# Kernel optimization log

Measured on AMD Instinct MI355X. Metric: run time of the kernel, lower is better.

Reference implementation:

```python
import jax, jax.numpy as jnp
import numpy as np

N_NODES = 50000
N_EDGES = 1600000
IN_FEAT = 128
OUT_FEAT = 128
NUM_RELS = 16
NUM_BASES = 4


def setup_inputs() -> dict:
    key = jax.random.key(0)
    ks = jax.random.split(key, 7)
    x = jax.random.normal(ks[0], (N_NODES, IN_FEAT), dtype=jnp.float32)
    W_bases = jax.random.normal(ks[1], (NUM_BASES, IN_FEAT, OUT_FEAT), dtype=jnp.float32) * (1.0 / np.sqrt(IN_FEAT))
    w_comp = jax.random.normal(ks[2], (NUM_RELS, NUM_BASES), dtype=jnp.float32)
    norm = jax.random.uniform(ks[3], (N_EDGES, 1), dtype=jnp.float32)
    src = jax.random.randint(ks[4], (N_EDGES,), 0, N_NODES, dtype=jnp.int32)
    dst = jax.random.randint(ks[5], (N_EDGES,), 0, N_NODES, dtype=jnp.int32)
    etype = jax.random.randint(ks[6], (N_EDGES,), 0, NUM_RELS, dtype=jnp.int32)
    return {"x": x, "W_bases": W_bases, "w_comp": w_comp, "norm": norm,
            "src": src, "dst": dst, "etype": etype}


def _combine_weights(W_bases, w_comp):
    # Faithful to the torch code: stack -> permute(1,0,2) -> matmul -> view(-1, out) -> split(in_feat)
    # [B, in, out] -> [in, B, out]
    Wb = jnp.transpose(W_bases, (1, 0, 2))
    # [R, B] @ [in, B, out] (batched over 'in') -> [in, R, out]
    W = jnp.matmul(w_comp, Wb)
    # view(-1, out) then split into chunks of in_feat rows == reshape(R, in, out)
    return W.reshape(-1, OUT_FEAT).reshape(NUM_RELS, IN_FEAT, OUT_FEAT)


def reference(x, W_bases, w_comp, norm, src, dst, etype):
    # per-relation weights [R, in, out]
    W = _combine_weights(W_bases, w_comp)
    # src_mul_edge: gather source node features, scale by per-edge norm  [E, in]
    msg = x[src] * norm
    # 'sum' aggregation per (relation, dst-node) segment  -> [R, N, in]
    seg = etype.astype(jnp.int32) * N_NODES + dst.astype(jnp.int32)
    agg = jax.ops.segment_sum(msg, seg, num_segments=NUM_RELS * N_NODES)
    agg = agg.reshape(NUM_RELS, N_NODES, IN_FEAT)
    # per-relation mm then merge across relation subgraphs with node_reduce 'sum'  -> [N, out]
    out = jnp.einsum('rni,rio->no', agg, W)
    # bias=None, activation=None in this configuration
    return out
```

## Files before the change

kernel.cpp:

```cpp
#include <hip/hip_runtime.h>


#define N_NODES  50000
#define N_EDGES  1600000
#define IN_FEAT  128
#define OUT_FEAT 128
#define NUM_RELS 16
#define NUM_BASES 4
#define XC_K     32
#define BIN_CAP  96
#define NPB      16
#define RS       516
#define ACCF_WORDS 8704

#define OFF_CNT      0
#define OFF_SPILLCNT 200000
#define OFF_SPILL    200064
#define OFF_BINS     6600064
#define OFF_XC       45000064
#define WS_NEED      51400064

__global__ __launch_bounds__(256) void prep(
    const float* __restrict__ x, const float* __restrict__ w_comp,
    const int* __restrict__ src, const int* __restrict__ dst,
    const int* __restrict__ etype, const float* __restrict__ norm,
    float* __restrict__ xc, int* __restrict__ cnt, uint2* __restrict__ bins,
    int* __restrict__ spillcnt, int* __restrict__ spill)
{
  {
    const int lane = threadIdx.x & 31;
    const int grp  = threadIdx.x >> 5;
    const int j = lane & 7;
    const int b = lane >> 3;
    float wc[16];
    #pragma unroll
    for (int t = 0; t < 16; ++t) wc[t] = w_comp[t * NUM_BASES + b];
    for (int n = blockIdx.x * 8 + grp; n < N_NODES; n += 2048 * 8) {
      const float4* xr = (const float4*)(x + (size_t)n * IN_FEAT) + j * 4;
      float acc = 0.f;
      #pragma unroll
      for (int q = 0; q < 4; ++q) {
        float4 v = xr[q];
        acc += v.x * wc[q*4+0] + v.y * wc[q*4+1]
             + v.z * wc[q*4+2] + v.w * wc[q*4+3];
      }
      xc[n * XC_K + lane] = acc;
    }
  }
  {
    const int e4 = (blockIdx.x * 256 + threadIdx.x) * 4;
    if (e4 < N_EDGES) {
      const int4   s4 = *(const int4*)&src[e4];
      const int4   d4 = *(const int4*)&dst[e4];
      const int4   t4 = *(const int4*)&etype[e4];
      const float4 n4 = *(const float4*)&norm[e4];
      const int   ss[4] = {s4.x, s4.y, s4.z, s4.w};
      const int   dd[4] = {d4.x, d4.y, d4.z, d4.w};
      const int   tt[4] = {t4.x, t4.y, t4.z, t4.w};
      const float nn[4] = {n4.x, n4.y, n4.z, n4.w};
      #pragma unroll
      for (int q = 0; q < 4; ++q) {
        const int pos = atomicAdd(&cnt[dd[q]], 1);
        if (pos < BIN_CAP) {
          bins[(size_t)dd[q] * BIN_CAP + pos] =
              make_uint2((unsigned)ss[q] | ((unsigned)tt[q] << 17),
                         __float_as_uint(nn[q]));
        } else {
          const int k = atomicAdd(spillcnt, 1);
          if (k < N_EDGES) spill[k] = e4 + q;
        }
      }
    }
  }
}

__device__ inline void red_write(float* accf, int slot, float4 (&ac)[4][2]) {
  const int base = slot * 34;
  #pragma unroll
  for (int nn = 0; nn < 4; ++nn) {
    *(float2*)&accf[base + nn*8 + 0] = make_float2(ac[nn][0].x, ac[nn][0].y);
    *(float2*)&accf[base + nn*8 + 2] = make_float2(ac[nn][0].z, ac[nn][0].w);
    *(float2*)&accf[base + nn*8 + 4] = make_float2(ac[nn][1].x, ac[nn][1].y);
    *(float2*)&accf[base + nn*8 + 6] = make_float2(ac[nn][1].z, ac[nn][1].w);
  }
}
__device__ inline void red_read(const float* accf, int slot, float4 (&ac)[4][2]) {
  const int base = slot * 34;
  #pragma unroll
  for (int nn = 0; nn < 4; ++nn) {
    float2 v0 = *(const float2*)&accf[base + nn*8 + 0];
    float2 v1 = *(const float2*)&accf[base + nn*8 + 2];
    float2 v2 = *(const float2*)&accf[base + nn*8 + 4];
    float2 v3 = *(const float2*)&accf[base + nn*8 + 6];
    ac[nn][0].x += v0.x; ac[nn][0].y += v0.y;
    ac[nn][0].z += v1.x; ac[nn][0].w += v1.y;
    ac[nn][1].x += v2.x; ac[nn][1].y += v2.y;
    ac[nn][1].z += v3.x; ac[nn][1].w += v3.y;
  }
}

__device__ inline float selb(const float4& v, int bb) {
  return bb == 0 ? v.x : bb == 1 ? v.y : bb == 2 ? v.z : v.w;
}

__global__ __launch_bounds__(512, 8) void rgcn_fused(
    const int* __restrict__ cnt, const uint2* __restrict__ bins,
    const float* __restrict__ xc, const float* __restrict__ Wb,
    float* __restrict__ out)
{
  __shared__ float accf[ACCF_WORDS];

  const int t    = threadIdx.x;
  const int w    = t >> 6;
  const int lane = t & 63;
  const int h    = lane >> 5;
  const int l5   = lane & 31;
  const int perm = (l5 & 7) * 4 + (l5 >> 3);

  for (int i = t; i < ACCF_WORDS / 4; i += 512)
    ((float4*)accf)[i] = make_float4(0.f, 0.f, 0.f, 0.f);
  __syncthreads();

  const int nodeBase = blockIdx.x * NPB;
  const int ln = w * 2 + h;
  const int n  = nodeBase + ln;
  int c = cnt[n]; c = c > BIN_CAP ? BIN_CAP : c;
  const int cmax   = max(c, __shfl_xor(c, 32));
  const int npairs = (cmax + 1) >> 1;

  const uint4* bp4 = (const uint4*)(bins + (size_t)n * BIN_CAP);
  const int awb = ln * RS + perm;

  uint4 q0 = bp4[0];
  int s00 = (0 < c) ? (int)(q0.x & 0x1FFFF) : 0;
  int s01 = (1 < c) ? (int)(q0.z & 0x1FFFF) : 0;
  float xa = xc[(size_t)s00 * XC_K + l5];
  float xb = xc[(size_t)s01 * XC_K + l5];
  uint4 q1 = bp4[1];

  for (int p = 0; p < npairs; ++p) {
    const int i0 = 2 * (p + 1);
    const int s10 = (i0     < c) ? (int)(q1.x & 0x1FFFF) : 0;
    const int s11 = (i0 + 1 < c) ? (int)(q1.z & 0x1FFFF) : 0;
    const float ya = xc[(size_t)s10 * XC_K + l5];
    const float yb = xc[(size_t)s11 * XC_K + l5];
    const uint4 q2 = bp4[p + 2];
    const int e0 = 2 * p;
    const float v0 = (e0     < c) ? xa * __uint_as_float(q0.y) : 0.f;
    const float v1 = (e0 + 1 < c) ? xb * __uint_as_float(q0.w) : 0.f;
    const int et0 = (int)((q0.x >> 17) & 15);
    const int et1 = (int)((q0.z >> 17) & 15);
    accf[awb + et0 * 32] += v0;
    accf[awb + et1 * 32] += v1;
    q0 = q1; q1 = q2; xa = ya; xb = yb;
  }
  __syncthreads();

  const int ks = w;
  const int ng = lane & 3;
  const int og = lane >> 2;
  const float* wbase = Wb + og * 8;

  float4 ac[4][2];
  #pragma unroll
  for (int nn = 0; nn < 4; ++nn) {
    ac[nn][0] = make_float4(0.f, 0.f, 0.f, 0.f);
    ac[nn][1] = make_float4(0.f, 0.f, 0.f, 0.f);
  }

  #pragma unroll 4
  for (int q = 0; q < 16; ++q) {
    const int k0 = ks * 64 + q * 4;
    const int r0 = (k0 >> 5) * 8 + ((k0 >> 2) & 7);
    float4 a4[4];
    #pragma unroll
    for (int nn = 0; nn < 4; ++nn)
      a4[nn] = *(const float4*)&accf[(ng * 4 + nn) * RS + k0];
    #pragma unroll
    for (int bb = 0; bb < 4; ++bb) {
      const float* wr = wbase + (size_t)(bb * 128 + r0) * 128;
      const float4 w0 = *(const float4*)wr;
      const float4 w1 = *(const float4*)(wr + 4);
      #pragma unroll
      for (int nn = 0; nn < 4; ++nn) {
        const float s = selb(a4[nn], bb);
        ac[nn][0].x += s * w0.x; ac[nn][0].y += s * w0.y;
        ac[nn][0].z += s * w0.z; ac[nn][0].w += s * w0.w;
        ac[nn][1].x += s * w1.x; ac[nn][1].y += s * w1.y;
        ac[nn][1].z += s * w1.z; ac[nn][1].w += s * w1.w;
      }
    }
  }

  __syncthreads();
  if (ks >= 4)             red_write(accf, (ks - 4) * 64 + lane, ac);
  __syncthreads();
  if (ks < 4)              red_read (accf, ks * 64 + lane, ac);
  __syncthreads();
  if (ks == 2 || ks == 3)  red_write(accf, (ks - 2) * 64 + lane, ac);
  __syncthreads();
  if (ks < 2)              red_read (accf, ks * 64 + lane, ac);
  __syncthreads();
  if (ks == 1)             red_write(accf, lane, ac);
  __syncthreads();
  if (ks == 0) {
    red_read(accf, lane, ac);
    #pragma unroll
    for (int nn = 0; nn < 4; ++nn) {
      const int node = nodeBase + ng * 4 + nn;
      *(float4*)(out + (size_t)node * OUT_FEAT + og * 8)     = ac[nn][0];
      *(float4*)(out + (size_t)node * OUT_FEAT + og * 8 + 4) = ac[nn][1];
    }
  }
}

__global__ __launch_bounds__(256) void spill_fix(
    const int* __restrict__ spillcnt, const int* __restrict__ spill,
    const float* __restrict__ xc, const float* __restrict__ Wb,
    const float* __restrict__ norm, const int* __restrict__ src,
    const int* __restrict__ dst, const int* __restrict__ etype,
    float* __restrict__ out)
{
  int cntv = *spillcnt; if (cntv > N_EDGES) cntv = N_EDGES;
  for (int idx = blockIdx.x * blockDim.x + threadIdx.x; idx < cntv;
       idx += gridDim.x * blockDim.x) {
    const int e = spill[idx];
    const int s = src[e], d = dst[e], et = etype[e];
    const float nm = norm[e];
    float m[32];
    #pragma unroll
    for (int l = 0; l < 32; ++l) m[l] = xc[(size_t)s * XC_K + l] * nm;
    for (int o = 0; o < OUT_FEAT; ++o) {
      float a = 0.f;
      #pragma unroll
      for (int l = 0; l < 32; ++l)
        a += m[l] * Wb[(size_t)((l >> 3) * 128 + et * 8 + (l & 7)) * OUT_FEAT + o];
      atomicAdd(&out[(size_t)d * OUT_FEAT + o], a);
    }
  }
}

__global__ __launch_bounds__(256) void edge_direct(
    const float* __restrict__ x, const float* __restrict__ W_bases,
    const float* __restrict__ w_comp, const float* __restrict__ norm,
    const int* __restrict__ src, const int* __restrict__ dst,
    const int* __restrict__ etype, float* __restrict__ out)
{
  const int wave = threadIdx.x >> 6;
  const int lane = threadIdx.x & 63;
  const int j = lane & 7;
  const int b = (lane >> 3) & 3;
  float wc[16];
  #pragma unroll
  for (int t = 0; t < 16; ++t) wc[t] = w_comp[t * NUM_BASES + b];
  for (int e = blockIdx.x * 4 + wave; e < N_EDGES; e += gridDim.x * 4) {
    const int s = src[e], d = dst[e], et = etype[e];
    const float nm = norm[e];
    const float4* xr = (const float4*)(x + (size_t)s * IN_FEAT) + j * 4;
    float m = 0.f;
    #pragma unroll
    for (int q = 0; q < 4; ++q) {
      float4 v = xr[q];
      m += v.x * wc[q*4+0] + v.y * wc[q*4+1]
         + v.z * wc[q*4+2] + v.w * wc[q*4+3];
    }
    m *= nm;
    float acc0 = 0.f, acc1 = 0.f;
    #pragma unroll
    for (int p = 0; p < 32; ++p) {
      float mv = __shfl(m, p, 64);
      const float* Wr = W_bases + (size_t)((p >> 3) * 128 + et * 8 + (p & 7)) * OUT_FEAT;
      acc0 += mv * Wr[lane];
      acc1 += mv * Wr[64 + lane];
    }
    atomicAdd(out + (size_t)d * OUT_FEAT + lane, acc0);
    atomicAdd(out + (size_t)d * OUT_FEAT + 64 + lane, acc1);
  }
}

extern "C" void kernel_launch(void* const* d_in, const int* in_sizes, int n_in,
                              void* d_out, int out_size, void* d_ws, size_t ws_size,
                              hipStream_t stream) {
  const float* x       = (const float*)d_in[0];
  const float* W_bases = (const float*)d_in[1];
  const float* w_comp  = (const float*)d_in[2];
  const float* norm    = (const float*)d_in[3];
  const int*   src     = (const int*)d_in[4];
  const int*   dst     = (const int*)d_in[5];
  const int*   etype   = (const int*)d_in[6];
  float* out = (float*)d_out;

  if (ws_size >= (size_t)WS_NEED) {
    char* ws = (char*)d_ws;
    int*   cntp     = (int*)(ws + OFF_CNT);
    int*   spillcnt = (int*)(ws + OFF_SPILLCNT);
    int*   spill    = (int*)(ws + OFF_SPILL);
    uint2* bins     = (uint2*)(ws + OFF_BINS);
    float* xc       = (float*)(ws + OFF_XC);

    hipMemsetAsync(cntp, 0, 200064, stream);
    prep<<<2048, 256, 0, stream>>>(x, w_comp, src, dst, etype, norm,
                                   xc, cntp, bins, spillcnt, spill);
    rgcn_fused<<<N_NODES / NPB, 512, 0, stream>>>(cntp, bins, xc, W_bases, out);
    spill_fix<<<16, 256, 0, stream>>>(spillcnt, spill, xc, W_bases,
                                      norm, src, dst, etype, out);
  } else {
    hipMemsetAsync(out, 0, (size_t)out_size * sizeof(float), stream);
    edge_direct<<<8192, 256, 0, stream>>>(x, W_bases, w_comp, norm,
                                          src, dst, etype, out);
  }
}
```

Measured before the change: 451.8 us.

## Split prep into separate kernels and deepen edge gather pipeline to four edges

The combined prep kernel is split into a node-precompute kernel with one block per 8 nodes and a separate edge-binning kernel, so each has a right-sized grid instead of one 2048-block grid with a grid-stride loop. The per-node edge loop in the fused kernel now handles four edges per iteration with a one-group lookahead, issuing four xc gathers at a time to hide memory latency. Source indices are clamped to valid nodes rather than masked by count. The cost is an extra kernel launch, more registers in the fused kernel, and extra bin reads past the count.

```diff
diff --git a/kernel.cpp b/kernel.cpp
--- a/kernel.cpp
+++ b/kernel.cpp
@@ -20,55 +20,57 @@
 #define OFF_XC       45000064
 #define WS_NEED      51400064
 
-__global__ __launch_bounds__(256) void prep(
+__global__ __launch_bounds__(256) void precomp_k(
     const float* __restrict__ x, const float* __restrict__ w_comp,
+    float* __restrict__ xc)
+{
+  const int lane = threadIdx.x & 31;
+  const int grp  = threadIdx.x >> 5;
+  const int j = lane & 7;
+  const int b = lane >> 3;
+  float wc[16];
+  #pragma unroll
+  for (int t = 0; t < 16; ++t) wc[t] = w_comp[t * NUM_BASES + b];
+  const int n = blockIdx.x * 8 + grp;
+  if (n < N_NODES) {
+    const float4* xr = (const float4*)(x + (size_t)n * IN_FEAT) + j * 4;
+    float acc = 0.f;
+    #pragma unroll
+    for (int q = 0; q < 4; ++q) {
+      float4 v = xr[q];
+      acc += v.x * wc[q*4+0] + v.y * wc[q*4+1]
+           + v.z * wc[q*4+2] + v.w * wc[q*4+3];
+    }
+    xc[n * XC_K + lane] = acc;
+  }
+}
+
+__global__ __launch_bounds__(256) void bin_k(
     const int* __restrict__ src, const int* __restrict__ dst,
     const int* __restrict__ etype, const float* __restrict__ norm,
-    float* __restrict__ xc, int* __restrict__ cnt, uint2* __restrict__ bins,
+    int* __restrict__ cnt, uint2* __restrict__ bins,
     int* __restrict__ spillcnt, int* __restrict__ spill)
 {
-  {
-    const int lane = threadIdx.x & 31;
-    const int grp  = threadIdx.x >> 5;
-    const int j = lane & 7;
-    const int b = lane >> 3;
-    float wc[16];
-    #pragma unroll
-    for (int t = 0; t < 16; ++t) wc[t] = w_comp[t * NUM_BASES + b];
-    for (int n = blockIdx.x * 8 + grp; n < N_NODES; n += 2048 * 8) {
-      const float4* xr = (const float4*)(x + (size_t)n * IN_FEAT) + j * 4;
-      float acc = 0.f;
-      #pragma unroll
-      for (int q = 0; q < 4; ++q) {
-        float4 v = xr[q];
-        acc += v.x * wc[q*4+0] + v.y * wc[q*4+1]
-             + v.z * wc[q*4+2] + v.w * wc[q*4+3];
-      }
-      xc[n * XC_K + lane] = acc;
-    }
-  }
-  {
-    const int e4 = (blockIdx.x * 256 + threadIdx.x) * 4;
-    if (e4 < N_EDGES) {
-      const int4   s4 = *(const int4*)&src[e4];
-      const int4   d4 = *(const int4*)&dst[e4];
-      const int4   t4 = *(const int4*)&etype[e4];
-      const float4 n4 = *(const float4*)&norm[e4];
-      const int   ss[4] = {s4.x, s4.y, s4.z, s4.w};
-      const int   dd[4] = {d4.x, d4.y, d4.z, d4.w};
-      const int   tt[4] = {t4.x, t4.y, t4.z, t4.w};
-      const float nn[4] = {n4.x, n4.y, n4.z, n4.w};
-      #pragma unroll
-      for (int q = 0; q < 4; ++q) {
-        const int pos = atomicAdd(&cnt[dd[q]], 1);
-        if (pos < BIN_CAP) {
-          bins[(size_t)dd[q] * BIN_CAP + pos] =
-              make_uint2((unsigned)ss[q] | ((unsigned)tt[q] << 17),
-                         __float_as_uint(nn[q]));
-        } else {
-          const int k = atomicAdd(spillcnt, 1);
-          if (k < N_EDGES) spill[k] = e4 + q;
-        }
+  const int e4 = (blockIdx.x * 256 + threadIdx.x) * 4;
+  if (e4 < N_EDGES) {
+    const int4   s4 = *(const int4*)&src[e4];
+    const int4   d4 = *(const int4*)&dst[e4];
+    const int4   t4 = *(const int4*)&etype[e4];
+    const float4 n4 = *(const float4*)&norm[e4];
+    const int   ss[4] = {s4.x, s4.y, s4.z, s4.w};
+    const int   dd[4] = {d4.x, d4.y, d4.z, d4.w};
+    const int   tt[4] = {t4.x, t4.y, t4.z, t4.w};
+    const float nn[4] = {n4.x, n4.y, n4.z, n4.w};
+    #pragma unroll
+    for (int q = 0; q < 4; ++q) {
+      const int pos = atomicAdd(&cnt[dd[q]], 1);
+      if (pos < BIN_CAP) {
+        bins[(size_t)dd[q] * BIN_CAP + pos] =
+            make_uint2((unsigned)ss[q] | ((unsigned)tt[q] << 17),
+                       __float_as_uint(nn[q]));
+      } else {
+        const int k = atomicAdd(spillcnt, 1);
+        if (k < N_EDGES) spill[k] = e4 + q;
       }
     }
   }
@@ -103,6 +105,11 @@
   return bb == 0 ? v.x : bb == 1 ? v.y : bb == 2 ? v.z : v.w;
 }
 
+__device__ inline unsigned clampsrc(unsigned v) {
+  unsigned s = v & 0x1FFFFu;
+  return s < (unsigned)N_NODES ? s : 0u;
+}
+
 __global__ __launch_bounds__(512, 8) void rgcn_fused(
     const int* __restrict__ cnt, const uint2* __restrict__ bins,
     const float* __restrict__ xc, const float* __restrict__ Wb,
@@ -125,34 +132,40 @@
   const int ln = w * 2 + h;
   const int n  = nodeBase + ln;
   int c = cnt[n]; c = c > BIN_CAP ? BIN_CAP : c;
-  const int cmax   = max(c, __shfl_xor(c, 32));
-  const int npairs = (cmax + 1) >> 1;
+  const int cmax    = max(c, __shfl_xor(c, 32));
+  const int ngroups = (cmax + 3) >> 2;
 
   const uint4* bp4 = (const uint4*)(bins + (size_t)n * BIN_CAP);
   const int awb = ln * RS + perm;
 
-  uint4 q0 = bp4[0];
-  int s00 = (0 < c) ? (int)(q0.x & 0x1FFFF) : 0;
-  int s01 = (1 < c) ? (int)(q0.z & 0x1FFFF) : 0;
-  float xa = xc[(size_t)s00 * XC_K + l5];
-  float xb = xc[(size_t)s01 * XC_K + l5];
-  uint4 q1 = bp4[1];
-
-  for (int p = 0; p < npairs; ++p) {
-    const int i0 = 2 * (p + 1);
-    const int s10 = (i0     < c) ? (int)(q1.x & 0x1FFFF) : 0;
-    const int s11 = (i0 + 1 < c) ? (int)(q1.z & 0x1FFFF) : 0;
-    const float ya = xc[(size_t)s10 * XC_K + l5];
-    const float yb = xc[(size_t)s11 * XC_K + l5];
-    const uint4 q2 = bp4[p + 2];
-    const int e0 = 2 * p;
-    const float v0 = (e0     < c) ? xa * __uint_as_float(q0.y) : 0.f;
-    const float v1 = (e0 + 1 < c) ? xb * __uint_as_float(q0.w) : 0.f;
-    const int et0 = (int)((q0.x >> 17) & 15);
-    const int et1 = (int)((q0.z >> 17) & 15);
-    accf[awb + et0 * 32] += v0;
-    accf[awb + et1 * 32] += v1;
-    q0 = q1; q1 = q2; xa = ya; xb = yb;
+  if (ngroups > 0) {
+    uint4 m0a = bp4[0], m0b = bp4[1];
+    uint4 m1a = bp4[2], m1b = bp4[3];
+    float x0 = xc[(size_t)clampsrc(m0a.x) * XC_K + l5];
+    float x1 = xc[(size_t)clampsrc(m0a.z) * XC_K + l5];
+    float x2 = xc[(size_t)clampsrc(m0b.x) * XC_K + l5];
+    float x3 = xc[(size_t)clampsrc(m0b.z) * XC_K + l5];
+
+    #pragma unroll 2
+    for (int g = 0; g < ngroups; ++g) {
+      const uint4 pa = bp4[2 * g + 4];
+      const uint4 pb = bp4[2 * g + 5];
+      const float y0 = xc[(size_t)clampsrc(m1a.x) * XC_K + l5];
+      const float y1 = xc[(size_t)clampsrc(m1a.z) * XC_K + l5];
+      const float y2 = xc[(size_t)clampsrc(m1b.x) * XC_K + l5];
+      const float y3 = xc[(size_t)clampsrc(m1b.z) * XC_K + l5];
+      const int e0 = 4 * g;
+      const float v0 = (e0     < c) ? __uint_as_float(m0a.y) : 0.f;
+      const float v1 = (e0 + 1 < c) ? __uint_as_float(m0a.w) : 0.f;
+      const float v2 = (e0 + 2 < c) ? __uint_as_float(m0b.y) : 0.f;
+      const float v3 = (e0 + 3 < c) ? __uint_as_float(m0b.w) : 0.f;
+      accf[awb + (int)((m0a.x >> 17) & 15) * 32] += x0 * v0;
+      accf[awb + (int)((m0a.z >> 17) & 15) * 32] += x1 * v1;
+      accf[awb + (int)((m0b.x >> 17) & 15) * 32] += x2 * v2;
+      accf[awb + (int)((m0b.z >> 17) & 15) * 32] += x3 * v3;
+      m0a = m1a; m0b = m1b; m1a = pa; m1b = pb;
+      x0 = y0; x1 = y1; x2 = y2; x3 = y3;
+    }
   }
   __syncthreads();
 
@@ -299,8 +312,9 @@
     float* xc       = (float*)(ws + OFF_XC);
 
     hipMemsetAsync(cntp, 0, 200064, stream);
-    prep<<<2048, 256, 0, stream>>>(x, w_comp, src, dst, etype, norm,
-                                   xc, cntp, bins, spillcnt, spill);
+    precomp_k<<<6250, 256, 0, stream>>>(x, w_comp, xc);
+    bin_k<<<1563, 256, 0, stream>>>(src, dst, etype, norm,
+                                    cntp, bins, spillcnt, spill);
     rgcn_fused<<<N_NODES / NPB, 512, 0, stream>>>(cntp, bins, xc, W_bases, out);
     spill_fix<<<16, 256, 0, stream>>>(spillcnt, spill, xc, W_bases,
                                       norm, src, dst, etype, out);
```

Result: no change. 455.7 us (+0.9%).
